# Performance work log

Hardware: AMD Instinct MI355X
Metric: run time of the kernel (lower is better)

Reference implementation:

```python
import jax, jax.numpy as jnp
import numpy as np

K = 40  # kNN neighbors (num_points arg)
B, N = 4, 4096

def _bn(x, g, b, axes):
    # training-mode BatchNorm over all axes except channel axis 1
    m = jnp.mean(x, axes, keepdims=True)
    v = jnp.var(x, axes, keepdims=True)
    sh = [1] * x.ndim
    sh[1] = -1
    return (x - m) / jnp.sqrt(v + 1e-5) * g.reshape(sh) + b.reshape(sh)

def _knn(x, k):
    # x: [B, C, N] -> idx [B, N, k]; same math as torch: topk of -||xi-xj||^2
    xx = jnp.sum(x * x, axis=1)                       # [B, N]
    inner = jnp.einsum('bcn,bcm->bnm', x, x)          # [B, N, N]
    neg_d2 = 2.0 * inner - xx[:, :, None] - xx[:, None, :]
    return jax.lax.top_k(neg_d2, k)[1]

def _graph_feature(x, k):
    # EdgeConv feature: concat(neighbor - center, center) -> [B, 2C, N, k]
    idx = jax.lax.stop_gradient(_knn(x, k))           # torch computes idx under no_grad
    xt = jnp.transpose(x, (0, 2, 1))                  # [B, N, C]
    nbr = jax.vmap(lambda f, i: f[i])(xt, idx)        # [B, N, k, C] gather
    ctr = xt[:, :, None, :]
    feat = jnp.concatenate([nbr - ctr, jnp.broadcast_to(ctr, nbr.shape)], axis=-1)
    return jnp.transpose(feat, (0, 3, 1, 2))

def _edge_block(x, W, b, g, e):
    f = _graph_feature(x, K)
    h = jnp.einsum('bcnk,oc->bonk', f, W) + b[None, :, None, None]  # 1x1 Conv2d
    h = jax.nn.leaky_relu(_bn(h, g, e, (0, 2, 3)), 0.2)
    return jnp.max(h, axis=-1)                        # max over k neighbors -> [B, Cout, N]

def _forward(x, w1, b1, g1, e1, w2, b2, g2, e2, w3, b3, g3, e3, w4, b4, g4, e4,
             w5, b5, g5, e5, tw, tb, tg, te, f1w, f1b, f1g, f1e,
             f2w, f2b, f2g, f2e, f3w, f3b):
    x1 = _edge_block(x,  w1, b1, g1, e1)              # [B,64,N]
    x2 = _edge_block(x1, w2, b2, g2, e2)              # [B,64,N]
    x3 = _edge_block(x2, w3, b3, g3, e3)              # [B,128,N]
    x4 = _edge_block(x3, w4, b4, g4, e4)              # [B,256,N]
    cat = jnp.concatenate([x1, x2, x3, x4], axis=1)   # [B,512,N]
    feat = jax.nn.leaky_relu(
        _bn(jnp.einsum('bcn,oc->bon', cat, w5) + b5[None, :, None], g5, e5, (0, 2)), 0.2)
    # TRANS head: Conv1d(1024,1024) -> global max -> MLP 1024-512-256-12 -> 4x4
    h = jax.nn.relu(_bn(jnp.einsum('bcn,oc->bon', feat, tw) + tb[None, :, None], tg, te, (0, 2)))
    h = jnp.max(h, axis=2)                            # [B,1024]
    h = jax.nn.relu(_bn(h @ f1w.T + f1b, f1g, f1e, (0,)))
    h = jax.nn.relu(_bn(h @ f2w.T + f2b, f2g, f2e, (0,)))
    h = h @ f3w.T + f3b                               # [B,12]
    iden = jnp.array([1, 0, 0, 0, 0, 1, 0, 0, 0, 0, 1, 0], jnp.float32)
    h = h + iden[None, :]
    app = jnp.broadcast_to(jnp.array([0, 0, 0, 1], jnp.float32)[None, :], (h.shape[0], 4))
    return jnp.concatenate([h, app], axis=1).reshape(-1, 4, 4)


def setup_inputs() -> dict:
    key = jax.random.key(0)
    ks = jax.random.split(key, 16)
    f32 = jnp.float32
    def W(i, shape, s=0.05):
        return jax.random.normal(ks[i], shape, f32) * s
    def bn_p(c):
        return jnp.ones(c, f32), jnp.zeros(c, f32)
    g1, e1 = bn_p(64); g2, e2 = bn_p(64); g3, e3 = bn_p(128); g4, e4 = bn_p(256)
    g5, e5 = bn_p(1024); tg, te = bn_p(1024); f1g, f1e = bn_p(512); f2g, f2e = bn_p(256)
    return {
        'x': jax.random.normal(ks[0], (B, 3, N), f32),
        'w1': W(1, (64, 6)),    'b1': jnp.zeros(64, f32),  'g1': g1, 'e1': e1,
        'w2': W(2, (64, 128)),  'b2': jnp.zeros(64, f32),  'g2': g2, 'e2': e2,
        'w3': W(3, (128, 128)), 'b3': jnp.zeros(128, f32), 'g3': g3, 'e3': e3,
        'w4': W(4, (256, 256)), 'b4': jnp.zeros(256, f32), 'g4': g4, 'e4': e4,
        'w5': W(5, (1024, 512)), 'b5': jnp.zeros(1024, f32), 'g5': g5, 'e5': e5,
        'tw': W(6, (1024, 1024)), 'tb': jnp.zeros(1024, f32), 'tg': tg, 'te': te,
        'f1w': W(7, (512, 1024)), 'f1b': jnp.zeros(512, f32), 'f1g': f1g, 'f1e': f1e,
        'f2w': W(8, (256, 512)),  'f2b': jnp.zeros(256, f32), 'f2g': f2g, 'f2e': f2e,
        'f3w': W(9, (12, 256)),   'f3b': jnp.zeros(12, f32),
    }


def reference(x, w1, b1, g1, e1, w2, b2, g2, e2, w3, b3, g3, e3, w4, b4, g4, e4,
              w5, b5, g5, e5, tw, tb, tg, te, f1w, f1b, f1g, f1e,
              f2w, f2b, f2g, f2e, f3w, f3b):
    return _forward(x, w1, b1, g1, e1, w2, b2, g2, e2, w3, b3, g3, e3, w4, b4, g4, e4,
                    w5, b5, g5, e5, tw, tb, tg, te, f1w, f1b, f1g, f1e,
                    f2w, f2b, f2g, f2e, f3w, f3b)
```

## Files before the change

### kernel.cpp

```cpp
#include <hip/hip_runtime.h>

#define BB 4
#define NN 4096
#define KK 40

#define NEG_FLT (-3.402823466e38f)
#define POS_FLT (3.402823466e38f)

typedef __attribute__((ext_vector_type(8))) short short8;
typedef __attribute__((ext_vector_type(4))) float f32x4;

__device__ __forceinline__ float lrelu02(float v){ return v > 0.f ? v : 0.2f*v; }
__device__ __forceinline__ int f2ord(float f){ int u = __float_as_int(f); return u >= 0 ? u : (u ^ 0x7fffffff); }
__device__ __forceinline__ unsigned ordu(float f){
  unsigned u = __float_as_uint(f);
  return (u & 0x80000000u) ? ~u : (u | 0x80000000u);
}
__device__ __forceinline__ unsigned long long packkey(float v, int m){
  return ((unsigned long long)ordu(v) << 32) | (unsigned)(~m);
}
__device__ __forceinline__ unsigned short f2bf(float f){
  unsigned u = __float_as_uint(f);
  unsigned r = u + 0x7fffu + ((u>>16)&1u);
  return (unsigned short)(r>>16);
}

template<int C>
__global__ void xx_kernel(const float* __restrict__ x, float* __restrict__ xx){
  int i = blockIdx.x*blockDim.x + threadIdx.x;
  if(i >= BB*NN) return;
  int b = i / NN, n = i % NN;
  const float* xb = x + (size_t)b*C*NN + n;
  float s = 0.f;
  #pragma unroll
  for(int c=0;c<C;c++){ float v = xb[(size_t)c*NN]; s += v*v; }
  xx[i] = s;
}

template<int C>
__global__ __launch_bounds__(256)
void dist_kernel(const float* __restrict__ xb, const float* __restrict__ xx,
                 float* __restrict__ dist){
  const int n0 = blockIdx.y*128, m0 = blockIdx.x*128;
  if(m0 < n0) return;
  __shared__ float As[16][132];
  __shared__ float Bs[16][132];
  const int tid = threadIdx.x;
  const int tx = tid & 15, ty = tid >> 4;
  const int lr = tid >> 4;
  const int lc0 = (tid & 15)*8;
  float acc[8][8] = {};
  for(int kt=0; kt<C; kt+=16){
    __syncthreads();
    {
      const float* an = xb + (size_t)(kt+lr)*NN + n0 + lc0;
      const float* am = xb + (size_t)(kt+lr)*NN + m0 + lc0;
      *(float4*)&As[lr][lc0]   = *(const float4*)an;
      *(float4*)&As[lr][lc0+4] = *(const float4*)(an+4);
      *(float4*)&Bs[lr][lc0]   = *(const float4*)am;
      *(float4*)&Bs[lr][lc0+4] = *(const float4*)(am+4);
    }
    __syncthreads();
    #pragma unroll
    for(int cc=0;cc<16;cc++){
      float a[8], b[8];
      *(float4*)&a[0] = *(const float4*)&As[cc][ty*8];
      *(float4*)&a[4] = *(const float4*)&As[cc][ty*8+4];
      *(float4*)&b[0] = *(const float4*)&Bs[cc][tx*8];
      *(float4*)&b[4] = *(const float4*)&Bs[cc][tx*8+4];
      #pragma unroll
      for(int i=0;i<8;i++)
        #pragma unroll
        for(int j=0;j<8;j++) acc[i][j] += a[i]*b[j];
    }
  }
  float xmv[8], xnv[8];
  #pragma unroll
  for(int j=0;j<8;j++) xmv[j] = xx[m0 + tx*8 + j];
  #pragma unroll
  for(int i=0;i<8;i++) xnv[i] = xx[n0 + ty*8 + i];
  #pragma unroll
  for(int i=0;i<8;i++){
    int n = n0 + ty*8 + i;
    float xn = xnv[i];
    float4 r0, r1;
    r0.x = 2.f*acc[i][0] - xn - xmv[0];
    r0.y = 2.f*acc[i][1] - xn - xmv[1];
    r0.z = 2.f*acc[i][2] - xn - xmv[2];
    r0.w = 2.f*acc[i][3] - xn - xmv[3];
    r1.x = 2.f*acc[i][4] - xn - xmv[4];
    r1.y = 2.f*acc[i][5] - xn - xmv[5];
    r1.z = 2.f*acc[i][6] - xn - xmv[6];
    r1.w = 2.f*acc[i][7] - xn - xmv[7];
    *(float4*)(dist + (size_t)n*NN + m0 + tx*8)     = r0;
    *(float4*)(dist + (size_t)n*NN + m0 + tx*8 + 4) = r1;
  }
  if(m0 != n0){
    #pragma unroll
    for(int j=0;j<8;j++){
      int m = m0 + tx*8 + j;
      float xm = xmv[j];
      float4 r0, r1;
      r0.x = 2.f*acc[0][j] - xnv[0] - xm;
      r0.y = 2.f*acc[1][j] - xnv[1] - xm;
      r0.z = 2.f*acc[2][j] - xnv[2] - xm;
      r0.w = 2.f*acc[3][j] - xnv[3] - xm;
      r1.x = 2.f*acc[4][j] - xnv[4] - xm;
      r1.y = 2.f*acc[5][j] - xnv[5] - xm;
      r1.z = 2.f*acc[6][j] - xnv[6] - xm;
      r1.w = 2.f*acc[7][j] - xnv[7] - xm;
      *(float4*)(dist + (size_t)m*NN + n0 + ty*8)     = r0;
      *(float4*)(dist + (size_t)m*NN + n0 + ty*8 + 4) = r1;
    }
  }
}

__global__ __launch_bounds__(256)
void dist3_kernel(const float* __restrict__ xb, const float* __restrict__ xx,
                  float* __restrict__ dist){
  int n = blockIdx.y;
  int m0 = (blockIdx.x*256 + threadIdx.x)*4;
  float c0 = xb[n], c1 = xb[NN+n], c2 = xb[2*NN+n];
  float xn = xx[n];
  float4 a = *(const float4*)(xb + m0);
  float4 b = *(const float4*)(xb + NN + m0);
  float4 c = *(const float4*)(xb + 2*NN + m0);
  float4 xm = *(const float4*)(xx + m0);
  float4 r;
  { float s = c0*a.x; s += c1*b.x; s += c2*c.x; r.x = 2.f*s - xn - xm.x; }
  { float s = c0*a.y; s += c1*b.y; s += c2*c.y; r.y = 2.f*s - xn - xm.y; }
  { float s = c0*a.z; s += c1*b.z; s += c2*c.z; r.z = 2.f*s - xn - xm.z; }
  { float s = c0*a.w; s += c1*b.w; s += c2*c.w; r.w = 2.f*s - xn - xm.w; }
  *(float4*)(dist + (size_t)n*NN + m0) = r;
}

#define INSQ(vf, mi) do{ \
  unsigned long long _pk = packkey((vf),(mi)); \
  if(_pk > t7){ \
    unsigned long long _lo; \
    _lo = _pk < t0 ? _pk : t0;  t0 = _pk > t0 ? _pk : t0;  _pk = _lo; \
    _lo = _pk < t1 ? _pk : t1;  t1 = _pk > t1 ? _pk : t1;  _pk = _lo; \
    _lo = _pk < t2 ? _pk : t2;  t2 = _pk > t2 ? _pk : t2;  _pk = _lo; \
    _lo = _pk < t3 ? _pk : t3;  t3 = _pk > t3 ? _pk : t3;  _pk = _lo; \
    _lo = _pk < t4 ? _pk : t4;  t4 = _pk > t4 ? _pk : t4;  _pk = _lo; \
    _lo = _pk < t5 ? _pk : t5;  t5 = _pk > t5 ? _pk : t5;  _pk = _lo; \
    _lo = _pk < t6 ? _pk : t6;  t6 = _pk > t6 ? _pk : t6;  _pk = _lo; \
    t7 = _pk > t7 ? _pk : t7; \
  } \
}while(0)

__global__ __launch_bounds__(256)
void select_kernel(const float* __restrict__ dA, const float* __restrict__ dB,
                   int* __restrict__ idx){
  const int wid = threadIdx.x >> 6;
  const int lane = threadIdx.x & 63;
  const int r = blockIdx.x*4 + wid;
  const float* row = (r < NN) ? (dA + (size_t)r*NN) : (dB + (size_t)(r-NN)*NN);

  unsigned long long t0=0,t1=0,t2=0,t3=0,t4=0,t5=0,t6=0,t7=0;
  unsigned long long done = 0ull;

  #pragma unroll 4
  for(int j=0;j<16;j++){
    float4 v = *(const float4*)(row + j*256 + lane*4);
    int mb = j*256 + lane*4;
    INSQ(v.x, mb+0); INSQ(v.y, mb+1); INSQ(v.z, mb+2); INSQ(v.w, mb+3);
  }

  __shared__ int outbuf[4][KK];
  #pragma unroll 1
  for(int k=0;k<KK;k++){
    unsigned long long wv = t0;
    #pragma unroll
    for(int off=32; off; off>>=1){
      unsigned long long ov = __shfl_xor(wv, off, 64);
      wv = ov > wv ? ov : wv;
    }
    int m = (int)(~(unsigned)wv);
    if(lane == ((m>>2)&63)){
      done |= 1ull << (((m>>8)<<2) | (m&3));
      t0=t1;t1=t2;t2=t3;t3=t4;t4=t5;t5=t6;t6=t7;t7=0;
      if(t0 == 0ull){
        #pragma unroll 1
        for(int j=0;j<16;j++){
          float4 v = *(const float4*)(row + j*256 + lane*4);
          int mb = j*256 + lane*4;
          if(!((done>>(j*4+0))&1)) INSQ(v.x, mb+0);
          if(!((done>>(j*4+1))&1)) INSQ(v.y, mb+1);
          if(!((done>>(j*4+2))&1)) INSQ(v.z, mb+2);
          if(!((done>>(j*4+3))&1)) INSQ(v.w, mb+3);
        }
      }
    }
    if(lane == 0) outbuf[wid][k] = m;
  }
  if(lane < KK) idx[(size_t)r*KK + lane] = outbuf[wid][lane];
}

template<int C, int O>
__global__ void wt_kernel(const float* __restrict__ w, float* __restrict__ Wt1,
                          float* __restrict__ Wtd){
  int i = blockIdx.x*256 + threadIdx.x;
  if(i >= C*O) return;
  int c = i / O, o = i % O;
  float a = w[(size_t)o*2*C + c];
  float b = w[(size_t)o*2*C + C + c];
  Wt1[i] = a; Wtd[i] = b - a;
}

template<int C, int O>
__global__ __launch_bounds__(256)
void pq_gemm_kernel(const float* __restrict__ x, const float* __restrict__ Wt1,
                    const float* __restrict__ Wtd, const float* __restrict__ bias,
                    float* __restrict__ P, float* __restrict__ Q){
  __shared__ float Xs[32][68];
  __shared__ float W1s[32][68];
  __shared__ float Wds[32][68];
  const int t0 = blockIdx.x*64;
  const int o0 = blockIdx.y*64;
  const int b  = t0 / NN, n0 = t0 % NN;
  const float* xb = x + (size_t)b*C*NN;
  const int tid = threadIdx.x;
  const int tx = tid & 15, ty = tid >> 4;
  const int lr = tid >> 3, lc0 = (tid & 7)*8;
  float pa[4][4] = {}, qa[4][4] = {};
  for(int kt=0; kt<C; kt+=32){
    __syncthreads();
    {
      const float* xs = xb + (size_t)(kt+lr)*NN + n0 + lc0;
      *(float4*)&Xs[lr][lc0]   = *(const float4*)xs;
      *(float4*)&Xs[lr][lc0+4] = *(const float4*)(xs+4);
      const float* w1 = Wt1 + (size_t)(kt+lr)*O + o0 + lc0;
      *(float4*)&W1s[lr][lc0]   = *(const float4*)w1;
      *(float4*)&W1s[lr][lc0+4] = *(const float4*)(w1+4);
      const float* wd = Wtd + (size_t)(kt+lr)*O + o0 + lc0;
      *(float4*)&Wds[lr][lc0]   = *(const float4*)wd;
      *(float4*)&Wds[lr][lc0+4] = *(const float4*)(wd+4);
    }
    __syncthreads();
    #pragma unroll
    for(int cc=0;cc<32;cc++){
      float a[4], w[4], d[4];
      *(float4*)a = *(const float4*)&Xs[cc][ty*4];
      *(float4*)w = *(const float4*)&W1s[cc][tx*4];
      *(float4*)d = *(const float4*)&Wds[cc][tx*4];
      #pragma unroll
      for(int i=0;i<4;i++)
        #pragma unroll
        for(int j=0;j<4;j++){
          pa[i][j] += a[i]*w[j];
          qa[i][j] += a[i]*d[j];
        }
    }
  }
  #pragma unroll
  for(int i=0;i<4;i++){
    size_t t = (size_t)t0 + ty*4 + i;
    #pragma unroll
    for(int j=0;j<4;j++){
      int o = o0 + tx*4 + j;
      P[t*O + o] = pa[i][j];
      Q[t*O + o] = qa[i][j] + bias[o];
    }
  }
}

template<int C, int O>
__global__ __launch_bounds__(256)
void pq_kernel(const float* __restrict__ x, const float* __restrict__ W,
               const float* __restrict__ bias,
               float* __restrict__ P, float* __restrict__ Q){
  constexpr int G = 256/O;
  constexpr int T = 8/G;
  constexpr int CP = ((C+3)/4)*4;
  __shared__ float xs[8][CP];
  const int tid = threadIdx.x;
  const long long t0b = (long long)blockIdx.x*8;
  const int b = (int)(t0b / NN), n0 = (int)(t0b % NN);
  const float* xb = x + (size_t)b*C*NN;
  for(int e=tid; e<8*C; e+=256){
    int tt = e / C, c = e % C;
    xs[tt][c] = xb[(size_t)c*NN + n0 + tt];
  }
  __syncthreads();

  const int o = tid % O, g = tid / O;
  const float* wrow = W + (size_t)o*2*C;
  float p[T], q[T];
  #pragma unroll
  for(int jt=0;jt<T;jt++){ p[jt]=0.f; q[jt]=0.f; }

  float w0=wrow[0], w1v=wrow[1], w2v=wrow[2];
  float d0=wrow[C+0]-w0, d1=wrow[C+1]-w1v, d2=wrow[C+2]-w2v;
  #pragma unroll
  for(int jt=0;jt<T;jt++){
    float a0=xs[g*T+jt][0], a1=xs[g*T+jt][1], a2=xs[g*T+jt][2];
    p[jt] += w0*a0; p[jt] += w1v*a1; p[jt] += w2v*a2;
    q[jt] += d0*a0; q[jt] += d1*a1; q[jt] += d2*a2;
  }
  float bv = bias[o];
  #pragma unroll
  for(int jt=0;jt<T;jt++){
    size_t t = (size_t)t0b + g*T + jt;
    P[t*O + o] = p[jt];
    Q[t*O + o] = q[jt] + bv;
  }
}

template<int O, int CH>
__global__ void edge_reduce_kernel(const float* __restrict__ P, const float* __restrict__ Q,
                                   const int* __restrict__ idx,
                                   float* __restrict__ maxh, float* __restrict__ minh,
                                   double* __restrict__ ssum, double* __restrict__ ssq){
  const int o = blockIdx.y*CH + threadIdx.x;
  const int TN = 8;
  int t0 = blockIdx.x*TN;
  double s = 0.0, s2 = 0.0;
  for(int t=t0;t<t0+TN;t++){
    int bbase = (t/NN)*NN;
    float q = Q[(size_t)t*O + o];
    const int* id = idx + (size_t)t*KK;
    float mx = NEG_FLT, mn = POS_FLT;
    for(int k=0;k<KK;k++){
      int m = id[k];
      float h = P[(size_t)(bbase+m)*O + o] + q;
      mx = fmaxf(mx, h); mn = fminf(mn, h);
      s += (double)h; s2 += (double)h*(double)h;
    }
    maxh[(size_t)t*O + o] = mx;
    minh[(size_t)t*O + o] = mn;
  }
  atomicAdd(&ssum[o], s);
  atomicAdd(&ssq[o], s2);
}

__global__ void finalize_stats(const double* __restrict__ ssum, const double* __restrict__ ssq,
                               const float* __restrict__ g, const float* __restrict__ beta,
                               float* __restrict__ scale, float* __restrict__ shift,
                               int O, double cnt){
  int o = blockIdx.x*blockDim.x + threadIdx.x;
  if(o >= O) return;
  double m = ssum[o]/cnt;
  double v = ssq[o]/cnt - m*m;
  if(v < 0.0) v = 0.0;
  float sc = g[o]/sqrtf((float)v + 1e-5f);
  scale[o] = sc;
  shift[o] = beta[o] - (float)m*sc;
}

template<int O>
__global__ void edge_apply_kernel(const float* __restrict__ maxh, const float* __restrict__ minh,
                                  const float* __restrict__ scale, const float* __restrict__ shift,
                                  float* __restrict__ xout, unsigned short* __restrict__ cat,
                                  int catOff){
  int i = blockIdx.x*blockDim.x + threadIdx.x;
  if(i >= BB*NN*O) return;
  int o = i % O; int t = i / O; int n = t % NN; int b = t / NN;
  float sc = scale[o];
  float v = sc >= 0.f ? maxh[i] : minh[i];
  float y = lrelu02(v*sc + shift[o]);
  xout[((size_t)b*O + o)*NN + n] = y;
  cat[(size_t)t*512 + catOff + o] = f2bf(y);
}

__global__ __launch_bounds__(256)
void gemm_bf16_kernel(const unsigned short* __restrict__ A, const unsigned short* __restrict__ Bw,
                      const float* __restrict__ bias, float* __restrict__ Cout,
                      int M, int Kd, int O){
  __shared__ unsigned short Al[128*72];
  __shared__ unsigned short Bl[128*72];
  const int m0 = blockIdx.x*128, o0 = blockIdx.y*128;
  const int tid = threadIdx.x;
  const int w = tid >> 6, l = tid & 63;
  const int wm = (w>>1)*64, wn = (w&1)*64;
  const int sr = tid >> 1;
  const int sc = (tid & 1)*32;
  const int frow = l & 15, kgrp = (l>>4)*8;
  f32x4 acc[4][4] = {};

  for(int kt=0; kt<Kd; kt+=64){
    const unsigned short* Ap = A  + (size_t)(m0+sr)*Kd + kt + sc;
    const unsigned short* Bp = Bw + (size_t)(o0+sr)*Kd + kt + sc;
    __syncthreads();
    *(short8*)&Al[sr*72 + sc     ] = *(const short8*)(Ap);
    *(short8*)&Al[sr*72 + sc +  8] = *(const short8*)(Ap+8);
    *(short8*)&Al[sr*72 + sc + 16] = *(const short8*)(Ap+16);
    *(short8*)&Al[sr*72 + sc + 24] = *(const short8*)(Ap+24);
    *(short8*)&Bl[sr*72 + sc     ] = *(const short8*)(Bp);
    *(short8*)&Bl[sr*72 + sc +  8] = *(const short8*)(Bp+8);
    *(short8*)&Bl[sr*72 + sc + 16] = *(const short8*)(Bp+16);
    *(short8*)&Bl[sr*72 + sc + 24] = *(const short8*)(Bp+24);
    __syncthreads();
    #pragma unroll
    for(int ks=0; ks<2; ks++){
      short8 af[4], bf[4];
      #pragma unroll
      for(int f=0; f<4; f++){
        af[f] = *(const short8*)&Al[(wm+f*16+frow)*72 + ks*32 + kgrp];
        bf[f] = *(const short8*)&Bl[(wn+f*16+frow)*72 + ks*32 + kgrp];
      }
      #pragma unroll
      for(int i=0;i<4;i++)
        #pragma unroll
        for(int j=0;j<4;j++)
          acc[i][j] = __builtin_amdgcn_mfma_f32_16x16x32_bf16(af[i], bf[j], acc[i][j], 0,0,0);
    }
  }
  const int crow = (l>>4)*4, ccol = l & 15;
  #pragma unroll
  for(int i=0;i<4;i++){
    #pragma unroll
    for(int j=0;j<4;j++){
      int oc = o0 + wn + j*16 + ccol;
      float bv = bias[oc];
      #pragma unroll
      for(int r=0;r<4;r++){
        int mr = m0 + wm + i*16 + crow + r;
        Cout[(size_t)mr*O + oc] = acc[i][j][r] + bv;
      }
    }
  }
}

__global__ void wcvt_kernel(const float* __restrict__ in, unsigned short* __restrict__ out, int n){
  int i = blockIdx.x*blockDim.x + threadIdx.x;
  if(i < n) out[i] = f2bf(in[i]);
}

__global__ void colstats_kernel(const float* __restrict__ H, double* __restrict__ ssum,
                                double* __restrict__ ssq, int O){
  int o  = blockIdx.x*blockDim.x + threadIdx.x;
  int m0 = blockIdx.y*64;
  double s=0.0, s2=0.0;
  for(int m=m0;m<m0+64;m++){
    float h = H[(size_t)m*O + o];
    s += (double)h; s2 += (double)h*(double)h;
  }
  atomicAdd(&ssum[o], s); atomicAdd(&ssq[o], s2);
}

__global__ void bn_lrelu_bf16_kernel(const float* __restrict__ H, const float* __restrict__ scale,
                                     const float* __restrict__ shift, unsigned short* __restrict__ Hb,
                                     int O, long long total){
  long long i = (long long)blockIdx.x*blockDim.x + threadIdx.x;
  if(i >= total) return;
  int o = (int)(i % O);
  Hb[i] = f2bf(lrelu02(H[i]*scale[o] + shift[o]));
}

__global__ void init_minmax_kernel(int* __restrict__ gmax, int* __restrict__ gmin, int n){
  int i = blockIdx.x*blockDim.x + threadIdx.x;
  if(i < n){ gmax[i] = -2147483647-1; gmin[i] = 2147483647; }
}

__global__ void colminmax_kernel(const float* __restrict__ H, int* __restrict__ gmax,
                                 int* __restrict__ gmin, int O){
  int o  = blockIdx.x*blockDim.x + threadIdx.x;
  int b  = blockIdx.y >> 4;
  int nt = blockIdx.y & 15;
  const float* Hp = H + (size_t)(b*NN + nt*256)*O + o;
  float mx = NEG_FLT, mn = POS_FLT;
  for(int i2=0;i2<256;i2++){
    float h = Hp[(size_t)i2*O];
    mx = fmaxf(mx, h); mn = fminf(mn, h);
  }
  atomicMax(&gmax[b*O + o], f2ord(mx));
  atomicMin(&gmin[b*O + o], f2ord(mn));
}

__global__ void t_apply_kernel(const int* __restrict__ gmax, const int* __restrict__ gmin,
                               const float* __restrict__ scale, const float* __restrict__ shift,
                               float* __restrict__ tfeat, int O){
  int i = blockIdx.x*blockDim.x + threadIdx.x;
  if(i >= BB*O) return;
  int o = i % O;
  float sc = scale[o];
  int ov = sc >= 0.f ? gmax[i] : gmin[i];
  float v = __int_as_float(ov >= 0 ? ov : (ov ^ 0x7fffffff));
  float y = v*sc + shift[o];
  tfeat[i] = fmaxf(y, 0.f);
}

__global__ __launch_bounds__(128)
void fc_bn_relu_kernel(const float* __restrict__ X, const float* __restrict__ W,
                       const float* __restrict__ bias, const float* __restrict__ g,
                       const float* __restrict__ beta, float* __restrict__ Y,
                       int Cin, int Cout){
  int j = blockIdx.x;
  __shared__ float red[4][128];
  float a0=0,a1=0,a2=0,a3=0;
  const float* w = W + (size_t)j*Cin;
  for(int c=threadIdx.x;c<Cin;c+=128){
    float wv = w[c];
    a0 += X[c]*wv; a1 += X[Cin+c]*wv; a2 += X[2*Cin+c]*wv; a3 += X[3*Cin+c]*wv;
  }
  red[0][threadIdx.x]=a0; red[1][threadIdx.x]=a1; red[2][threadIdx.x]=a2; red[3][threadIdx.x]=a3;
  __syncthreads();
  for(int s=64;s>=1;s>>=1){
    if(threadIdx.x < s){
      #pragma unroll
      for(int b=0;b<4;b++) red[b][threadIdx.x] += red[b][threadIdx.x+s];
    }
    __syncthreads();
  }
  if(threadIdx.x == 0){
    float h[4];
    #pragma unroll
    for(int b=0;b<4;b++) h[b] = red[b][0] + bias[j];
    float m = 0.25f*(h[0]+h[1]+h[2]+h[3]);
    float var = 0.f;
    #pragma unroll
    for(int b=0;b<4;b++){ float d = h[b]-m; var += d*d; }
    var *= 0.25f;
    float sc = g[j]/sqrtf(var + 1e-5f);
    #pragma unroll
    for(int b=0;b<4;b++){
      float y = (h[b]-m)*sc + beta[j];
      Y[(size_t)b*Cout + j] = fmaxf(y, 0.f);
    }
  }
}

__global__ __launch_bounds__(64)
void fc3_kernel(const float* __restrict__ X, const float* __restrict__ W,
                const float* __restrict__ bias, float* __restrict__ out){
  int t = threadIdx.x; int b = t >> 4; int j = t & 15;
  float v;
  if(j < 12){
    float acc = 0.f;
    const float* w = W + (size_t)j*256;
    const float* xb = X + (size_t)b*256;
    for(int c=0;c<256;c++) acc += xb[c]*w[c];
    v = acc + bias[j];
    if(j==0 || j==5 || j==10) v += 1.f;
  } else {
    v = (j==15) ? 1.f : 0.f;
  }
  out[t] = v;
}

template<int C>
static void run_knn(const float* xin, const float* xxb, float* distA, float* distB,
                    int* idxb, hipStream_t stream){
  for(int half=0; half<2; half++){
    int b0 = half*2;
    for(int j=0;j<2;j++){
      int b = b0 + j;
      float* dd = j==0 ? distA : distB;
      const float* xb = xin + (size_t)b*C*NN;
      const float* xx = xxb + (size_t)b*NN;
      if constexpr(C == 3){
        dist3_kernel<<<dim3(NN/1024, NN), 256, 0, stream>>>(xb, xx, dd);
      } else {
        dist_kernel<C><<<dim3(NN/128, NN/128), 256, 0, stream>>>(xb, xx, dd);
      }
    }
    select_kernel<<<2*NN/4, 256, 0, stream>>>(distA, distB, idxb + (size_t)b0*NN*KK);
  }
}

template<int C, int O>
static void run_edge_block(const float* xin, const float* W, const float* bias,
                           const float* g, const float* e, float* xout, int catOff,
                           float* xxb, int* idxb, float* P, float* Q,
                           float* maxh, float* minh, float* distB,
                           float* Wt1, float* Wtd,
                           double* ssum, double* ssq,
                           float* scaleb, float* shiftb, unsigned short* catb, hipStream_t stream){
  xx_kernel<C><<<(BB*NN+255)/256, 256, 0, stream>>>(xin, xxb);
  run_knn<C>(xin, xxb, P , distB, idxb, stream);
  if constexpr(C >= 32){
    wt_kernel<C,O><<<(C*O+255)/256, 256, 0, stream>>>(W, Wt1, Wtd);
    pq_gemm_kernel<C,O><<<dim3(BB*NN/64, O/64), 256, 0, stream>>>(xin, Wt1, Wtd, bias, P, Q);
  } else {
    pq_kernel<C,O><<<BB*NN/8, 256, 0, stream>>>(xin, W, bias, P, Q);
  }
  hipMemsetAsync(ssum, 0, O*sizeof(double), stream);
  hipMemsetAsync(ssq,  0, O*sizeof(double), stream);
  constexpr int CH = (O > 128) ? 128 : O;
  edge_reduce_kernel<O,CH><<<dim3(BB*NN/8, O/CH), CH, 0, stream>>>(P, Q, idxb, maxh, minh, ssum, ssq);
  finalize_stats<<<(O+255)/256, 256, 0, stream>>>(ssum, ssq, g, e, scaleb, shiftb, O, (double)BB*NN*KK);
  edge_apply_kernel<O><<<(BB*NN*O+255)/256, 256, 0, stream>>>(maxh, minh, scaleb, shiftb, xout, catb, catOff);
}

extern "C" void kernel_launch(void* const* d_in, const int* in_sizes, int n_in,
                              void* d_out, int out_size, void* d_ws, size_t ws_size,
                              hipStream_t stream){
  (void)in_sizes; (void)n_in; (void)out_size; (void)ws_size;
  const float* x   = (const float*)d_in[0];
  const float* w1  = (const float*)d_in[1];  const float* b1 = (const float*)d_in[2];
  const float* g1  = (const float*)d_in[3];  const float* e1 = (const float*)d_in[4];
  const float* w2  = (const float*)d_in[5];  const float* b2 = (const float*)d_in[6];
  const float* g2  = (const float*)d_in[7];  const float* e2 = (const float*)d_in[8];
  const float* w3  = (const float*)d_in[9];  const float* b3 = (const float*)d_in[10];
  const float* g3  = (const float*)d_in[11]; const float* e3 = (const float*)d_in[12];
  const float* w4  = (const float*)d_in[13]; const float* b4 = (const float*)d_in[14];
  const float* g4  = (const float*)d_in[15]; const float* e4 = (const float*)d_in[16];
  const float* w5  = (const float*)d_in[17]; const float* b5 = (const float*)d_in[18];
  const float* g5  = (const float*)d_in[19]; const float* e5 = (const float*)d_in[20];
  const float* twp = (const float*)d_in[21]; const float* tbp = (const float*)d_in[22];
  const float* tg  = (const float*)d_in[23]; const float* te  = (const float*)d_in[24];
  const float* f1w = (const float*)d_in[25]; const float* f1b = (const float*)d_in[26];
  const float* f1g = (const float*)d_in[27]; const float* f1e = (const float*)d_in[28];
  const float* f2w = (const float*)d_in[29]; const float* f2b = (const float*)d_in[30];
  const float* f2g = (const float*)d_in[31]; const float* f2e = (const float*)d_in[32];
  const float* f3w = (const float*)d_in[33]; const float* f3b = (const float*)d_in[34];

  char* ws = (char*)d_ws;
  size_t off = 0;
  auto alloc = [&](size_t bytes)->void*{
    void* p = ws + off;
    off += (bytes + 255) & ~(size_t)255;
    return p;
  };
  int*    idxb  = (int*)   alloc((size_t)BB*NN*KK*4);
  float*  xxb   = (float*) alloc((size_t)BB*NN*4);
  float*  x1    = (float*) alloc((size_t)BB*64*NN*4);
  float*  x2    = (float*) alloc((size_t)BB*64*NN*4);
  float*  x3    = (float*) alloc((size_t)BB*128*NN*4);
  float*  x4    = (float*) alloc((size_t)BB*256*NN*4);
  float*  P     = (float*) alloc((size_t)BB*NN*256*4);
  float*  Q     = (float*) alloc((size_t)BB*NN*256*4);
  float*  maxh  = (float*) alloc((size_t)BB*NN*256*4);
  float*  minh  = (float*) alloc((size_t)BB*NN*256*4);
  unsigned short* catb = (unsigned short*) alloc((size_t)BB*NN*512*2);
  float*  h5    = (float*) alloc((size_t)BB*NN*1024*4);
  float*  Wt1   = (float*) alloc((size_t)256*128*4);
  float*  Wtd   = (float*) alloc((size_t)256*128*4);
  double* ssum  = (double*)alloc(1024*8);
  double* ssq   = (double*)alloc(1024*8);
  float*  scaleb= (float*) alloc(1024*4);
  float*  shiftb= (float*) alloc(1024*4);
  int*    gmax  = (int*)   alloc((size_t)BB*1024*4);
  int*    gmin  = (int*)   alloc((size_t)BB*1024*4);
  float*  tfeat = (float*) alloc((size_t)BB*1024*4);
  float*  y1    = (float*) alloc((size_t)BB*512*4);
  float*  y2    = (float*) alloc((size_t)BB*256*4);

  unsigned short* w5b  = (unsigned short*)x1;
  unsigned short* twb  = (unsigned short*)x2;
  unsigned short* h5b  = (unsigned short*)maxh;
  float*          h6   = h5;

  run_edge_block<3,  64 >(x,  w1, b1, g1, e1, x1, 0,   xxb, idxb, P, Q, maxh, minh, h5, Wt1, Wtd, ssum, ssq, scaleb, shiftb, catb, stream);
  run_edge_block<64, 64 >(x1, w2, b2, g2, e2, x2, 64,  xxb, idxb, P, Q, maxh, minh, h5, Wt1, Wtd, ssum, ssq, scaleb, shiftb, catb, stream);
  run_edge_block<64, 128>(x2, w3, b3, g3, e3, x3, 128, xxb, idxb, P, Q, maxh, minh, h5, Wt1, Wtd, ssum, ssq, scaleb, shiftb, catb, stream);
  run_edge_block<128,256>(x3, w4, b4, g4, e4, x4, 256, xxb, idxb, P, Q, maxh, minh, h5, Wt1, Wtd, ssum, ssq, scaleb, shiftb, catb, stream);

  const int M = BB*NN;
  wcvt_kernel<<<(1024*512 +255)/256, 256, 0, stream>>>(w5,  w5b, 1024*512);
  wcvt_kernel<<<(1024*1024+255)/256, 256, 0, stream>>>(twp, twb, 1024*1024);

  gemm_bf16_kernel<<<dim3(M/128, 1024/128), 256, 0, stream>>>(catb, w5b, b5, h5, M, 512, 1024);
  hipMemsetAsync(ssum, 0, 1024*8, stream);
  hipMemsetAsync(ssq,  0, 1024*8, stream);
  colstats_kernel<<<dim3(1024/256, M/64), 256, 0, stream>>>(h5, ssum, ssq, 1024);
  finalize_stats<<<4, 256, 0, stream>>>(ssum, ssq, g5, e5, scaleb, shiftb, 1024, (double)M);
  bn_lrelu_bf16_kernel<<<(int)(((long long)M*1024+255)/256), 256, 0, stream>>>(h5, scaleb, shiftb, h5b, 1024, (long long)M*1024);

  gemm_bf16_kernel<<<dim3(M/128, 1024/128), 256, 0, stream>>>(h5b, twb, tbp, h6, M, 1024, 1024);
  hipMemsetAsync(ssum, 0, 1024*8, stream);
  hipMemsetAsync(ssq,  0, 1024*8, stream);
  init_minmax_kernel<<<(BB*1024+255)/256, 256, 0, stream>>>(gmax, gmin, BB*1024);
  colstats_kernel<<<dim3(1024/256, M/64), 256, 0, stream>>>(h6, ssum, ssq, 1024);
  colminmax_kernel<<<dim3(1024/256, BB*(NN/256)), 256, 0, stream>>>(h6, gmax, gmin, 1024);
  finalize_stats<<<4, 256, 0, stream>>>(ssum, ssq, tg, te, scaleb, shiftb, 1024, (double)M);
  t_apply_kernel<<<(BB*1024+255)/256, 256, 0, stream>>>(gmax, gmin, scaleb, shiftb, tfeat, 1024);

  fc_bn_relu_kernel<<<512, 128, 0, stream>>>(tfeat, f1w, f1b, f1g, f1e, y1, 1024, 512);
  fc_bn_relu_kernel<<<256, 128, 0, stream>>>(y1, f2w, f2b, f2g, f2e, y2, 512, 256);
  fc3_kernel<<<1, 64, 0, stream>>>(y2, f3w, f3b, (float*)d_out);
}
```

Baseline: 1.979 ms.

## Fuse 3-channel distance computation into kNN selection; widen edge reduce blocks

For the first edge block (C=3), the separate distance kernel that wrote a full N×N matrix is removed. A new select3 kernel computes distances on the fly inside the top-k selection and recomputes them during refills, which avoids the large global write and read-back. The edge reduce kernel now uses one block per point tile with O threads, instead of splitting channels across a second grid dimension. The trade-off is extra arithmetic on refill passes, plus 256-thread blocks for the O=256 layer.

```diff
diff --git a/kernel.cpp b/kernel.cpp
--- a/kernel.cpp
+++ b/kernel.cpp
@@ -115,25 +115,6 @@
   }
 }
 
-__global__ __launch_bounds__(256)
-void dist3_kernel(const float* __restrict__ xb, const float* __restrict__ xx,
-                  float* __restrict__ dist){
-  int n = blockIdx.y;
-  int m0 = (blockIdx.x*256 + threadIdx.x)*4;
-  float c0 = xb[n], c1 = xb[NN+n], c2 = xb[2*NN+n];
-  float xn = xx[n];
-  float4 a = *(const float4*)(xb + m0);
-  float4 b = *(const float4*)(xb + NN + m0);
-  float4 c = *(const float4*)(xb + 2*NN + m0);
-  float4 xm = *(const float4*)(xx + m0);
-  float4 r;
-  { float s = c0*a.x; s += c1*b.x; s += c2*c.x; r.x = 2.f*s - xn - xm.x; }
-  { float s = c0*a.y; s += c1*b.y; s += c2*c.y; r.y = 2.f*s - xn - xm.y; }
-  { float s = c0*a.z; s += c1*b.z; s += c2*c.z; r.z = 2.f*s - xn - xm.z; }
-  { float s = c0*a.w; s += c1*b.w; s += c2*c.w; r.w = 2.f*s - xn - xm.w; }
-  *(float4*)(dist + (size_t)n*NN + m0) = r;
-}
-
 #define INSQ(vf, mi) do{ \
   unsigned long long _pk = packkey((vf),(mi)); \
   if(_pk > t7){ \
@@ -189,6 +170,74 @@
           if(!((done>>(j*4+1))&1)) INSQ(v.y, mb+1);
           if(!((done>>(j*4+2))&1)) INSQ(v.z, mb+2);
           if(!((done>>(j*4+3))&1)) INSQ(v.w, mb+3);
+        }
+      }
+    }
+    if(lane == 0) outbuf[wid][k] = m;
+  }
+  if(lane < KK) idx[(size_t)r*KK + lane] = outbuf[wid][lane];
+}
+
+__global__ __launch_bounds__(256)
+void select3_kernel(const float* __restrict__ x, const float* __restrict__ xx,
+                    int* __restrict__ idx){
+  const int wid = threadIdx.x >> 6;
+  const int lane = threadIdx.x & 63;
+  const int r = blockIdx.x*4 + wid;
+  const int b = r / NN, n = r % NN;
+  const float* xb  = x + (size_t)b*3*NN;
+  const float* xxb = xx + (size_t)b*NN;
+  const float c0 = xb[n], c1 = xb[NN+n], c2 = xb[2*NN+n];
+  const float xn = xxb[n];
+
+  unsigned long long t0=0,t1=0,t2=0,t3=0,t4=0,t5=0,t6=0,t7=0;
+  unsigned long long done = 0ull;
+
+  #pragma unroll 4
+  for(int j=0;j<16;j++){
+    int mb = j*256 + lane*4;
+    float4 a  = *(const float4*)(xb + mb);
+    float4 bb = *(const float4*)(xb + NN + mb);
+    float4 c  = *(const float4*)(xb + 2*NN + mb);
+    float4 xm = *(const float4*)(xxb + mb);
+    float vx, vy, vz, vw;
+    { float s = c0*a.x; s += c1*bb.x; s += c2*c.x; vx = 2.f*s - xn - xm.x; }
+    { float s = c0*a.y; s += c1*bb.y; s += c2*c.y; vy = 2.f*s - xn - xm.y; }
+    { float s = c0*a.z; s += c1*bb.z; s += c2*c.z; vz = 2.f*s - xn - xm.z; }
+    { float s = c0*a.w; s += c1*bb.w; s += c2*c.w; vw = 2.f*s - xn - xm.w; }
+    INSQ(vx, mb+0); INSQ(vy, mb+1); INSQ(vz, mb+2); INSQ(vw, mb+3);
+  }
+
+  __shared__ int outbuf[4][KK];
+  #pragma unroll 1
+  for(int k=0;k<KK;k++){
+    unsigned long long wv = t0;
+    #pragma unroll
+    for(int off=32; off; off>>=1){
+      unsigned long long ov = __shfl_xor(wv, off, 64);
+      wv = ov > wv ? ov : wv;
+    }
+    int m = (int)(~(unsigned)wv);
+    if(lane == ((m>>2)&63)){
+      done |= 1ull << (((m>>8)<<2) | (m&3));
+      t0=t1;t1=t2;t2=t3;t3=t4;t4=t5;t5=t6;t6=t7;t7=0;
+      if(t0 == 0ull){
+        #pragma unroll 1
+        for(int j=0;j<16;j++){
+          int mb = j*256 + lane*4;
+          float4 a  = *(const float4*)(xb + mb);
+          float4 bb = *(const float4*)(xb + NN + mb);
+          float4 c  = *(const float4*)(xb + 2*NN + mb);
+          float4 xm = *(const float4*)(xxb + mb);
+          float vx, vy, vz, vw;
+          { float s = c0*a.x; s += c1*bb.x; s += c2*c.x; vx = 2.f*s - xn - xm.x; }
+          { float s = c0*a.y; s += c1*bb.y; s += c2*c.y; vy = 2.f*s - xn - xm.y; }
+          { float s = c0*a.z; s += c1*bb.z; s += c2*c.z; vz = 2.f*s - xn - xm.z; }
+          { float s = c0*a.w; s += c1*bb.w; s += c2*c.w; vw = 2.f*s - xn - xm.w; }
+          if(!((done>>(j*4+0))&1)) INSQ(vx, mb+0);
+          if(!((done>>(j*4+1))&1)) INSQ(vy, mb+1);
+          if(!((done>>(j*4+2))&1)) INSQ(vz, mb+2);
+          if(!((done>>(j*4+3))&1)) INSQ(vw, mb+3);
         }
       }
     }
@@ -307,12 +356,12 @@
   }
 }
 
-template<int O, int CH>
+template<int O>
 __global__ void edge_reduce_kernel(const float* __restrict__ P, const float* __restrict__ Q,
                                    const int* __restrict__ idx,
                                    float* __restrict__ maxh, float* __restrict__ minh,
                                    double* __restrict__ ssum, double* __restrict__ ssq){
-  const int o = blockIdx.y*CH + threadIdx.x;
+  const int o = threadIdx.x;
   const int TN = 8;
   int t0 = blockIdx.x*TN;
   double s = 0.0, s2 = 0.0;
@@ -542,20 +591,20 @@
 template<int C>
 static void run_knn(const float* xin, const float* xxb, float* distA, float* distB,
                     int* idxb, hipStream_t stream){
-  for(int half=0; half<2; half++){
-    int b0 = half*2;
-    for(int j=0;j<2;j++){
-      int b = b0 + j;
-      float* dd = j==0 ? distA : distB;
-      const float* xb = xin + (size_t)b*C*NN;
-      const float* xx = xxb + (size_t)b*NN;
-      if constexpr(C == 3){
-        dist3_kernel<<<dim3(NN/1024, NN), 256, 0, stream>>>(xb, xx, dd);
-      } else {
+  if constexpr(C == 3){
+    select3_kernel<<<BB*NN/4, 256, 0, stream>>>(xin, xxb, idxb);
+  } else {
+    for(int half=0; half<2; half++){
+      int b0 = half*2;
+      for(int j=0;j<2;j++){
+        int b = b0 + j;
+        float* dd = j==0 ? distA : distB;
+        const float* xb = xin + (size_t)b*C*NN;
+        const float* xx = xxb + (size_t)b*NN;
         dist_kernel<C><<<dim3(NN/128, NN/128), 256, 0, stream>>>(xb, xx, dd);
       }
-    }
-    select_kernel<<<2*NN/4, 256, 0, stream>>>(distA, distB, idxb + (size_t)b0*NN*KK);
+      select_kernel<<<2*NN/4, 256, 0, stream>>>(distA, distB, idxb + (size_t)b0*NN*KK);
+    }
   }
 }
 
@@ -577,8 +626,7 @@
   }
   hipMemsetAsync(ssum, 0, O*sizeof(double), stream);
   hipMemsetAsync(ssq,  0, O*sizeof(double), stream);
-  constexpr int CH = (O > 128) ? 128 : O;
-  edge_reduce_kernel<O,CH><<<dim3(BB*NN/8, O/CH), CH, 0, stream>>>(P, Q, idxb, maxh, minh, ssum, ssq);
+  edge_reduce_kernel<O><<<BB*NN/8, O, 0, stream>>>(P, Q, idxb, maxh, minh, ssum, ssq);
   finalize_stats<<<(O+255)/256, 256, 0, stream>>>(ssum, ssq, g, e, scaleb, shiftb, O, (double)BB*NN*KK);
   edge_apply_kernel<O><<<(BB*NN*O+255)/256, 256, 0, stream>>>(maxh, minh, scaleb, shiftb, xout, catb, catOff);
 }
```

New measurement: 1.887 ms. -4.6%, faster.
